# Performance work log

Hardware: AMD Instinct MI355X
Metric: run time of the kernel (lower is better)

Reference implementation:

```python
import jax, jax.numpy as jnp
import numpy as np

N_EMBD = 768
N_HEADS = 12
HEAD_DIM = N_EMBD // N_HEADS


def _layernorm(x):
    # LayerNorm without affine params, eps=1e-5 (torch default)
    mu = jnp.mean(x, axis=-1, keepdims=True)
    var = jnp.var(x, axis=-1, keepdims=True)
    return (x - mu) * jax.lax.rsqrt(var + 1e-5)


def setup_inputs() -> dict:
    key = jax.random.key(0)
    ks = jax.random.split(key, 6)
    B, T, C = 1, 4096, N_EMBD
    s = lambda fan_in: 1.0 / np.sqrt(fan_in)
    return {
        "x": jax.random.normal(ks[0], (B, T, C), jnp.float32),
        "W_kqv": jax.random.normal(ks[1], (C, 3 * C), jnp.float32) * s(C),
        "W_proj": jax.random.normal(ks[2], (C, C), jnp.float32) * s(C),
        "W_fc": jax.random.normal(ks[3], (C, 2 * C), jnp.float32) * s(C),
        "b_fc": jax.random.normal(ks[4], (2 * C,), jnp.float32) * s(C),
        "W_cproj": jax.random.normal(ks[5], (2 * C, C), jnp.float32) * s(2 * C),
    }


def _attention(h, W_kqv, W_proj):
    B, T, C = h.shape
    kqv = h @ W_kqv                       # (B, T, 3C)
    kqv = kqv.reshape(B, T, 3, N_HEADS, HEAD_DIM)
    k = kqv[:, :, 0]                      # (B, T, H, Dh) -- note k first, per source
    q = kqv[:, :, 1]
    v = kqv[:, :, 2]
    scale = HEAD_DIM ** -0.5
    scores = jnp.einsum('bqhd,bkhd->bhqk', q, k) * scale
    attn = jax.nn.softmax(scores, axis=-1)
    out = jnp.einsum('bhqk,bkhd->bqhd', attn, v).reshape(B, T, C)
    return out @ W_proj


def _mlp(h, W_fc, b_fc, W_cproj):
    h = h @ W_fc + b_fc
    h = jax.nn.gelu(h, approximate=False)  # torch nn.GELU default = exact erf
    return h @ W_cproj


def reference(x, W_kqv, W_proj, W_fc, b_fc, W_cproj):
    x = x + _attention(_layernorm(x), W_kqv, W_proj)
    x = x + _mlp(_layernorm(x), W_fc, b_fc, W_cproj)
    return x
```

## Files before the change

kernel.cpp:

```cpp
#include <hip/hip_runtime.h>
#include <hip/hip_bf16.h>
#include <math.h>

#define T_SEQ 4096
#define C_EMB 768
#define NHEAD 12
#define HDIM  64
#define NZ    2

typedef __bf16 bf16;
typedef __bf16 bf16x8 __attribute__((ext_vector_type(8)));
typedef __bf16 bf16x4 __attribute__((ext_vector_type(4)));
typedef float  f32x4  __attribute__((ext_vector_type(4)));
typedef float  f32x16 __attribute__((ext_vector_type(16)));

#if __has_builtin(__builtin_amdgcn_exp2f)
#define EXP2 __builtin_amdgcn_exp2f
#else
#define EXP2 exp2f
#endif


__device__ __forceinline__ void stage16(const void* g, void* ldsbase) {
  __builtin_amdgcn_global_load_lds(
      (__attribute__((address_space(1))) const unsigned int*)g,
      (__attribute__((address_space(3))) unsigned int*)ldsbase, 16, 0, 0);
}

__device__ __forceinline__ f32x16 zero16() {
  f32x16 z;
#pragma unroll
  for (int i = 0; i < 16; i++) z[i] = 0.f;
  return z;
}

__device__ __forceinline__ void do_transpose(const float* __restrict__ W,
                                             bf16* __restrict__ Wt, int K, int N,
                                             int bx, int by, int tid,
                                             float (*tile)[33]) {
  const int n0 = bx * 32, k0 = by * 32;
  const int tx = tid & 31, ty = tid >> 5;
#pragma unroll
  for (int i = 0; i < 32; i += 8)
    tile[ty + i][tx] = W[(size_t)(k0 + ty + i) * N + n0 + tx];
  __syncthreads();
#pragma unroll
  for (int i = 0; i < 32; i += 8)
    Wt[(size_t)(n0 + ty + i) * K + k0 + tx] = (bf16)tile[tx][ty + i];
}

__device__ __forceinline__ void do_ln(const float* __restrict__ x,
                                      bf16* __restrict__ y, int row, int t,
                                      float* red) {
  const float* xr = x + (size_t)row * C_EMB;
  float v0 = xr[t], v1 = xr[t + 256], v2 = xr[t + 512];
  float s  = v0 + v1 + v2;
  float ss = v0 * v0 + v1 * v1 + v2 * v2;
#pragma unroll
  for (int m = 1; m < 64; m <<= 1) {
    s += __shfl_xor(s, m);
    ss += __shfl_xor(ss, m);
  }
  const int w = t >> 6;
  if ((t & 63) == 0) { red[w] = s; red[4 + w] = ss; }
  __syncthreads();
  s  = red[0] + red[1] + red[2] + red[3];
  ss = red[4] + red[5] + red[6] + red[7];
  const float mu  = s * (1.0f / C_EMB);
  const float var = ss * (1.0f / C_EMB) - mu * mu;
  const float rs  = rsqrtf(var + 1e-5f);
  bf16* yr = y + (size_t)row * C_EMB;
  yr[t]       = (bf16)((v0 - mu) * rs);
  yr[t + 256] = (bf16)((v1 - mu) * rs);
  yr[t + 512] = (bf16)((v2 - mu) * rs);
}

__global__ void prep(const float* __restrict__ x, bf16* __restrict__ ln_out,
                     const float* __restrict__ W_kqv, bf16* __restrict__ Wkqv_t,
                     const float* __restrict__ W_proj, bf16* __restrict__ Wproj_t,
                     const float* __restrict__ W_fc, bf16* __restrict__ Wfc_t,
                     const float* __restrict__ W_cproj, bf16* __restrict__ Wcp_t) {
  __shared__ float tile[32][33];
  const int b = blockIdx.x, t = threadIdx.x;
  if (b < 1728) {
    do_transpose(W_kqv, Wkqv_t, 768, 2304, b % 72, b / 72, t, tile);
  } else if (b < 2304) {
    const int bb = b - 1728;
    do_transpose(W_proj, Wproj_t, 768, 768, bb % 24, bb / 24, t, tile);
  } else if (b < 3456) {
    const int bb = b - 2304;
    do_transpose(W_fc, Wfc_t, 768, 1536, bb % 48, bb / 48, t, tile);
  } else if (b < 4608) {
    const int bb = b - 3456;
    do_transpose(W_cproj, Wcp_t, 1536, 768, bb % 24, bb / 24, t, tile);
  } else {
    do_ln(x, ln_out, b - 4608, t, &tile[0][0]);
  }
}

__global__ void ln_rows(const bf16* __restrict__ x, bf16* __restrict__ y) {
  const int w = threadIdx.x >> 6, l = threadIdx.x & 63;
  const int row = blockIdx.x * 4 + w;
  const bf16* xr = x + (size_t)row * C_EMB;
  const bf16x8 v8 = *reinterpret_cast<const bf16x8*>(xr + l * 8);
  const bf16x4 v4 = *reinterpret_cast<const bf16x4*>(xr + 512 + l * 4);
  float f[12];
#pragma unroll
  for (int j = 0; j < 8; j++) f[j] = (float)v8[j];
#pragma unroll
  for (int j = 0; j < 4; j++) f[8 + j] = (float)v4[j];
  float s = 0.f, ss = 0.f;
#pragma unroll
  for (int j = 0; j < 12; j++) { s += f[j]; ss += f[j] * f[j]; }
#pragma unroll
  for (int m = 1; m < 64; m <<= 1) {
    s += __shfl_xor(s, m);
    ss += __shfl_xor(ss, m);
  }
  const float mu  = s * (1.0f / C_EMB);
  const float var = ss * (1.0f / C_EMB) - mu * mu;
  const float rs  = rsqrtf(var + 1e-5f);
  bf16x8 o8;
  bf16x4 o4;
#pragma unroll
  for (int j = 0; j < 8; j++) o8[j] = (bf16)((f[j] - mu) * rs);
#pragma unroll
  for (int j = 0; j < 4; j++) o4[j] = (bf16)((f[8 + j] - mu) * rs);
  bf16* yr = y + (size_t)row * C_EMB;
  *reinterpret_cast<bf16x8*>(yr + l * 8) = o8;
  *reinterpret_cast<bf16x4*>(yr + 512 + l * 4) = o4;
}

template <int EPI, int BM>
__global__ void gemm_bt(const bf16* __restrict__ A, const bf16* __restrict__ BT,
                        void* __restrict__ Cout, const void* __restrict__ res,
                        const float* __restrict__ bias, int M, int N, int K) {
  __shared__ __align__(16) bf16 As[BM * 64];
  __shared__ __align__(16) bf16 Bs[64 * 64];
  constexpr int MR = BM / 32;
  const int nrow = M / BM;
  const int ncol = N >> 6;
  const int rpx = nrow >> 3;
  const int bid = blockIdx.x;
  const int xcd = bid & 7, idx = bid >> 3;
  const int rowb = xcd * rpx + idx / ncol;
  const int colb = idx % ncol;
  const int row0 = rowb * BM, col0 = colb * 64;

  const int tid = threadIdx.x;
  const int w = tid >> 6, lane = tid & 63;
  const int wr = w >> 1, wc = w & 1;
  const int l15 = lane & 15, l4 = lane >> 4;

  f32x4 acc[MR][2];
#pragma unroll
  for (int m = 0; m < MR; m++)
#pragma unroll
    for (int n = 0; n < 2; n++) acc[m][n] = (f32x4){0.f, 0.f, 0.f, 0.f};

  const int rr = lane >> 3;
  const int c8 = (lane & 7) * 8;

  for (int k0 = 0; k0 < K; k0 += 64) {
    const bf16* gA = A + (size_t)(row0 + w * (BM / 4) + rr) * K + k0 + c8;
    const bf16* gB = BT + (size_t)(col0 + w * 16 + rr) * K + k0 + c8;
#pragma unroll
    for (int i = 0; i < BM / 32; i++)
      stage16(gA + (size_t)(8 * i) * K, As + (w * (BM / 4) + 8 * i) * 64);
#pragma unroll
    for (int i = 0; i < 2; i++)
      stage16(gB + (size_t)(8 * i) * K, Bs + (w * 16 + 8 * i) * 64);
    __syncthreads();

#pragma unroll
    for (int hh = 0; hh < 2; hh++) {
      bf16x8 af[MR], bfv[2];
#pragma unroll
      for (int m = 0; m < MR; m++)
        af[m] = *reinterpret_cast<const bf16x8*>(
            As + (wr * (BM / 2) + m * 16 + l15) * 64 + hh * 32 + l4 * 8);
#pragma unroll
      for (int n = 0; n < 2; n++)
        bfv[n] = *reinterpret_cast<const bf16x8*>(
            Bs + (wc * 32 + n * 16 + l15) * 64 + hh * 32 + l4 * 8);
#pragma unroll
      for (int m = 0; m < MR; m++)
#pragma unroll
        for (int n = 0; n < 2; n++)
          acc[m][n] = __builtin_amdgcn_mfma_f32_16x16x32_bf16(af[m], bfv[n], acc[m][n], 0, 0, 0);
    }
    __syncthreads();
  }

  const int orow = row0 + wr * (BM / 2);
  const int ocol = col0 + wc * 32;
#pragma unroll
  for (int m = 0; m < MR; m++) {
#pragma unroll
    for (int n = 0; n < 2; n++) {
      const int c = ocol + n * 16 + l15;
#pragma unroll
      for (int j = 0; j < 4; j++) {
        const int r = orow + m * 16 + l4 * 4 + j;
        const size_t idx2 = (size_t)r * N + c;
        const float v = acc[m][n][j];
        if (EPI == 0) {
          ((bf16*)Cout)[idx2] = (bf16)v;
        } else if (EPI == 1) {
          ((bf16*)Cout)[idx2] = (bf16)(((const float*)res)[idx2] + v);
        } else if (EPI == 2) {
          const float h = v + bias[c];
          ((bf16*)Cout)[idx2] = (bf16)(0.5f * h * (1.0f + erff(h * 0.70710678118f)));
        } else if (EPI == 3) {
          ((float*)Cout)[idx2] = (float)((const bf16*)res)[idx2] + v;
        } else {
          const float sc = (c >= 768 && c < 1536) ? 0.18033688011112042f : 1.0f;
          ((bf16*)Cout)[idx2] = (bf16)(v * sc);
        }
      }
    }
  }
}

__global__ __launch_bounds__(256, 3)
void attn_fused(const bf16* __restrict__ kqv,
                bf16* __restrict__ Opart,
                float* __restrict__ Lpart) {
  const int fid = blockIdx.x;
  const int xs = fid & 7, r = fid >> 3;
  const int qb = r & 31;
  const int s = xs * 3 + (r >> 5);
  const int h = s % 12, z = s / 12;
  const int tid = threadIdx.x, w = tid >> 6, lane = tid & 63;
  const int l31 = lane & 31, hi = lane >> 5;

  __shared__ __align__(16) char KsB[128 * 144];
  __shared__ __align__(16) char VtB[64 * 272];

  const int qrow = qb * 128 + w * 32 + l31;
  const bf16* qp = kqv + (size_t)qrow * 2304 + 768 + h * 64;
  bf16x8 qf[4];
#pragma unroll
  for (int m = 0; m < 4; m++)
    qf[m] = *reinterpret_cast<const bf16x8*>(qp + hi * 8 + 16 * m);

  bf16x8 ones;
#pragma unroll
  for (int e = 0; e < 8; e++) ones[e] = (bf16)1.0f;

  f32x16 accO0 = zero16(), accO1 = zero16(), accL = zero16();

  const int krow = tid >> 1;
  const int kc0 = (tid & 1) * 4;
  const int kb = tid & 31, db = tid >> 5;
  const int lb = ((kb >> 3) & 3) * 32 + ((kb >> 2) & 1) * 16 + (kb & 1) * 8 +
                 ((kb >> 1) & 1) * 4;

  const int kt0 = z * 16;

  bf16x8 kreg[4], vreg[4];
#define LOADKV(kt)                                                               \
  {                                                                              \
    const bf16* kp =                                                             \
        kqv + (size_t)((kt)*128 + krow) * 2304 + h * 64 + kc0 * 8;               \
    _Pragma("unroll") for (int i = 0; i < 4; i++)                                \
        kreg[i] = *reinterpret_cast<const bf16x8*>(kp + i * 8);                  \
    const bf16* vp =                                                             \
        kqv + (size_t)((kt)*128 + kb * 4) * 2304 + 1536 + h * 64 + db * 8;       \
    _Pragma("unroll") for (int r2 = 0; r2 < 4; r2++)                             \
        vreg[r2] = *reinterpret_cast<const bf16x8*>(vp + (size_t)r2 * 2304);     \
  }

  LOADKV(kt0);

  for (int kt = 0; kt < 16; kt++) {
    __syncthreads();
    {
      char* kdst = KsB + krow * 144;
#pragma unroll
      for (int i = 0; i < 4; i++)
        *reinterpret_cast<bf16x8*>(kdst + ((kc0 + i) * 16)) = kreg[i];
#pragma unroll
      for (int e = 0; e < 8; e++) {
        const int d = db * 8 + e;
        const bf16x4 pk4 = (bf16x4){vreg[0][e], vreg[1][e], vreg[2][e], vreg[3][e]};
        *reinterpret_cast<bf16x4*>(VtB + d * 272 + lb * 2) = pk4;
      }
    }
    __syncthreads();
    if (kt + 1 < 16) LOADKV(kt0 + kt + 1);

    __builtin_amdgcn_s_setprio(1);

    bf16x8 pb[8];
#pragma unroll
    for (int t = 0; t < 4; t++) {
      f32x16 st = zero16();
#pragma unroll
      for (int m = 0; m < 4; m++) {
        const bf16x8 kf = *reinterpret_cast<const bf16x8*>(
            KsB + (size_t)(32 * t + l31) * 144 + (2 * m + hi) * 16);
        st = __builtin_amdgcn_mfma_f32_32x32x16_bf16(kf, qf[m], st, 0, 0, 0);
      }
#pragma unroll
      for (int hf = 0; hf < 2; hf++) {
        bf16x8 p;
#pragma unroll
        for (int j = 0; j < 8; j++) p[j] = (bf16)EXP2(st[hf * 8 + j]);
        pb[2 * t + hf] = p;
      }
    }

#pragma unroll
    for (int mk = 0; mk < 8; mk++) {
      const bf16x8 vf0 = *reinterpret_cast<const bf16x8*>(
          VtB + (size_t)l31 * 272 + (2 * mk + hi) * 16);
      accO0 = __builtin_amdgcn_mfma_f32_32x32x16_bf16(vf0, pb[mk], accO0, 0, 0, 0);
      const bf16x8 vf1 = *reinterpret_cast<const bf16x8*>(
          VtB + (size_t)(32 + l31) * 272 + (2 * mk + hi) * 16);
      accO1 = __builtin_amdgcn_mfma_f32_32x32x16_bf16(vf1, pb[mk], accO1, 0, 0, 0);
      accL = __builtin_amdgcn_mfma_f32_32x32x16_bf16(ones, pb[mk], accL, 0, 0, 0);
    }

    __builtin_amdgcn_s_setprio(0);
  }
#undef LOADKV

  bf16* Oq = Opart + (size_t)z * T_SEQ * C_EMB + (size_t)qrow * C_EMB + h * 64;
#pragma unroll
  for (int s4 = 0; s4 < 4; s4++) {
    const bf16x4 o0 = (bf16x4){(bf16)accO0[4 * s4 + 0], (bf16)accO0[4 * s4 + 1],
                               (bf16)accO0[4 * s4 + 2], (bf16)accO0[4 * s4 + 3]};
    *reinterpret_cast<bf16x4*>(Oq + 8 * s4 + 4 * hi) = o0;
    const bf16x4 o1 = (bf16x4){(bf16)accO1[4 * s4 + 0], (bf16)accO1[4 * s4 + 1],
                               (bf16)accO1[4 * s4 + 2], (bf16)accO1[4 * s4 + 3]};
    *reinterpret_cast<bf16x4*>(Oq + 32 + 8 * s4 + 4 * hi) = o1;
  }
  if (hi == 0)
    Lpart[(size_t)z * NHEAD * T_SEQ + (size_t)h * T_SEQ + qrow] = accL[0];
}

__global__ void attn_combine(const bf16* __restrict__ Opart,
                             const float* __restrict__ Lpart,
                             bf16* __restrict__ out) {
  const int t = threadIdx.x;
  const int rr = t / 96, cc = t % 96;
  const int q = blockIdx.x * 4 + rr;
  const int c = cc * 8;
  const int h = c >> 6;
  float o[8];
#pragma unroll
  for (int j = 0; j < 8; j++) o[j] = 0.f;
  float L = 0.f;
#pragma unroll
  for (int z = 0; z < NZ; z++) {
    const bf16x8 v = *reinterpret_cast<const bf16x8*>(
        Opart + (size_t)z * T_SEQ * C_EMB + (size_t)q * C_EMB + c);
#pragma unroll
    for (int j = 0; j < 8; j++) o[j] += (float)v[j];
    L += Lpart[(size_t)z * NHEAD * T_SEQ + (size_t)h * T_SEQ + q];
  }
  const float inv = 1.0f / L;
  bf16x8 rv;
#pragma unroll
  for (int j = 0; j < 8; j++) rv[j] = (bf16)(o[j] * inv);
  *reinterpret_cast<bf16x8*>(out + (size_t)q * C_EMB + c) = rv;
}

extern "C" void kernel_launch(void* const* d_in, const int* in_sizes, int n_in,
                              void* d_out, int out_size, void* d_ws, size_t ws_size,
                              hipStream_t stream) {
  const float* x       = (const float*)d_in[0];
  const float* W_kqv   = (const float*)d_in[1];
  const float* W_proj  = (const float*)d_in[2];
  const float* W_fc    = (const float*)d_in[3];
  const float* b_fc    = (const float*)d_in[4];
  const float* W_cproj = (const float*)d_in[5];
  float* outp = (float*)d_out;

  char* p = (char*)d_ws;
  bf16* Wkqv_t  = (bf16*)p; p += (size_t)2304 * 768 * 2;
  bf16* Wproj_t = (bf16*)p; p += (size_t)768 * 768 * 2;
  bf16* Wfc_t   = (bf16*)p; p += (size_t)1536 * 768 * 2;
  bf16* Wcp_t   = (bf16*)p; p += (size_t)768 * 1536 * 2;
  bf16* A1      = (bf16*)p; p += (size_t)4096 * 768 * 2;
  bf16* KQV     = (bf16*)p; p += (size_t)4096 * 2304 * 2;
  bf16* x1      = (bf16*)p; p += (size_t)4096 * 768 * 2;
  bf16* Opart   = (bf16*)p; p += (size_t)NZ * 4096 * 768 * 2;
  float* Lpart  = (float*)p; p += (size_t)NZ * NHEAD * 4096 * 4;
  bf16* attn_o = A1;
  bf16* A2     = KQV;
  bf16* Hg     = KQV + (size_t)4096 * 768;

  prep<<<8704, 256, 0, stream>>>(x, A1, W_kqv, Wkqv_t, W_proj, Wproj_t,
                                 W_fc, Wfc_t, W_cproj, Wcp_t);
  gemm_bt<4, 128><<<1152, 256, 0, stream>>>(A1, Wkqv_t, KQV, nullptr, nullptr,
                                            4096, 2304, 768);
  attn_fused<<<768, 256, 0, stream>>>(KQV, Opart, Lpart);
  attn_combine<<<1024, 384, 0, stream>>>(Opart, Lpart, attn_o);
  gemm_bt<1, 64><<<768, 256, 0, stream>>>(attn_o, Wproj_t, x1, x, nullptr,
                                          4096, 768, 768);
  ln_rows<<<1024, 256, 0, stream>>>(x1, A2);
  gemm_bt<2, 64><<<1536, 256, 0, stream>>>(A2, Wfc_t, Hg, nullptr, b_fc,
                                           4096, 1536, 768);
  gemm_bt<3, 64><<<768, 256, 0, stream>>>(Hg, Wcp_t, outp, x1, nullptr,
                                          4096, 768, 1536);
}
```

Measured before the change: 178.3 us.

## Fuse attention split-combine into output projection GEMM prologue

Removes the separate attn_combine kernel and writes a dedicated projection GEMM that loads both partial attention outputs and their softmax denominators, sums and normalizes them while staging the A tile into LDS. This drops one launch and a full write and read of the combined attention output. In exchange the A operand is now loaded synchronously through registers rather than the async LDS path, and the new kernel has no double buffering, so the GEMM main loop may stall more.

New measurement: 178.0 us. Within noise of the previous version (-0.2%).

```diff
diff --git a/kernel.cpp b/kernel.cpp
--- a/kernel.cpp
+++ b/kernel.cpp
@@ -206,8 +206,6 @@
         const float v = acc[m][n][j];
         if (EPI == 0) {
           ((bf16*)Cout)[idx2] = (bf16)v;
-        } else if (EPI == 1) {
-          ((bf16*)Cout)[idx2] = (bf16)(((const float*)res)[idx2] + v);
         } else if (EPI == 2) {
           const float h = v + bias[c];
           ((bf16*)Cout)[idx2] = (bf16)(0.5f * h * (1.0f + erff(h * 0.70710678118f)));
@@ -217,6 +215,96 @@
           const float sc = (c >= 768 && c < 1536) ? 0.18033688011112042f : 1.0f;
           ((bf16*)Cout)[idx2] = (bf16)(v * sc);
         }
+      }
+    }
+  }
+}
+
+__global__ void gemm_proj(const bf16* __restrict__ Opart,
+                          const float* __restrict__ Lpart,
+                          const bf16* __restrict__ BT,
+                          bf16* __restrict__ Cout,
+                          const float* __restrict__ res) {
+  constexpr int M = 4096, N = 768, K = 768;
+  __shared__ __align__(16) bf16 As[64 * 64];
+  __shared__ __align__(16) bf16 Bs[64 * 64];
+  const int bid = blockIdx.x;
+  const int xcd = bid & 7, idx = bid >> 3;
+  const int rowb = xcd * 8 + idx / 12;
+  const int colb = idx % 12;
+  const int row0 = rowb * 64, col0 = colb * 64;
+
+  const int tid = threadIdx.x;
+  const int w = tid >> 6, lane = tid & 63;
+  const int wr = w >> 1, wc = w & 1;
+  const int l15 = lane & 15, l4 = lane >> 4;
+
+  f32x4 acc[2][2];
+#pragma unroll
+  for (int m = 0; m < 2; m++)
+#pragma unroll
+    for (int n = 0; n < 2; n++) acc[m][n] = (f32x4){0.f, 0.f, 0.f, 0.f};
+
+  const int rr = lane >> 3;
+  const int c8 = (lane & 7) * 8;
+
+  for (int k0 = 0; k0 < K; k0 += 64) {
+    const int h = k0 >> 6;
+#pragma unroll
+    for (int i = 0; i < 2; i++) {
+      const int ar = row0 + w * 16 + 8 * i + rr;
+      const float L =
+          Lpart[(size_t)h * T_SEQ + ar] +
+          Lpart[(size_t)NHEAD * T_SEQ + (size_t)h * T_SEQ + ar];
+      const float inv = 1.0f / L;
+      const bf16x8 o0 = *reinterpret_cast<const bf16x8*>(
+          Opart + (size_t)ar * C_EMB + k0 + c8);
+      const bf16x8 o1 = *reinterpret_cast<const bf16x8*>(
+          Opart + (size_t)T_SEQ * C_EMB + (size_t)ar * C_EMB + k0 + c8);
+      bf16x8 av;
+#pragma unroll
+      for (int j = 0; j < 8; j++)
+        av[j] = (bf16)(((float)o0[j] + (float)o1[j]) * inv);
+      *reinterpret_cast<bf16x8*>(As + (w * 16 + 8 * i + rr) * 64 + c8) = av;
+    }
+    const bf16* gB = BT + (size_t)(col0 + w * 16 + rr) * K + k0 + c8;
+#pragma unroll
+    for (int i = 0; i < 2; i++)
+      stage16(gB + (size_t)(8 * i) * K, Bs + (w * 16 + 8 * i) * 64);
+    __syncthreads();
+
+#pragma unroll
+    for (int hh = 0; hh < 2; hh++) {
+      bf16x8 af[2], bfv[2];
+#pragma unroll
+      for (int m = 0; m < 2; m++)
+        af[m] = *reinterpret_cast<const bf16x8*>(
+            As + (wr * 32 + m * 16 + l15) * 64 + hh * 32 + l4 * 8);
+#pragma unroll
+      for (int n = 0; n < 2; n++)
+        bfv[n] = *reinterpret_cast<const bf16x8*>(
+            Bs + (wc * 32 + n * 16 + l15) * 64 + hh * 32 + l4 * 8);
+#pragma unroll
+      for (int m = 0; m < 2; m++)
+#pragma unroll
+        for (int n = 0; n < 2; n++)
+          acc[m][n] = __builtin_amdgcn_mfma_f32_16x16x32_bf16(af[m], bfv[n], acc[m][n], 0, 0, 0);
+    }
+    __syncthreads();
+  }
+
+  const int orow = row0 + wr * 32;
+  const int ocol = col0 + wc * 32;
+#pragma unroll
+  for (int m = 0; m < 2; m++) {
+#pragma unroll
+    for (int n = 0; n < 2; n++) {
+      const int c = ocol + n * 16 + l15;
+#pragma unroll
+      for (int j = 0; j < 4; j++) {
+        const int r = orow + m * 16 + l4 * 4 + j;
+        const size_t idx2 = (size_t)r * N + c;
+        Cout[idx2] = (bf16)(res[idx2] + acc[m][n][j]);
       }
     }
   }
@@ -340,33 +428,6 @@
     Lpart[(size_t)z * NHEAD * T_SEQ + (size_t)h * T_SEQ + qrow] = accL[0];
 }
 
-__global__ void attn_combine(const bf16* __restrict__ Opart,
-                             const float* __restrict__ Lpart,
-                             bf16* __restrict__ out) {
-  const int t = threadIdx.x;
-  const int rr = t / 96, cc = t % 96;
-  const int q = blockIdx.x * 4 + rr;
-  const int c = cc * 8;
-  const int h = c >> 6;
-  float o[8];
-#pragma unroll
-  for (int j = 0; j < 8; j++) o[j] = 0.f;
-  float L = 0.f;
-#pragma unroll
-  for (int z = 0; z < NZ; z++) {
-    const bf16x8 v = *reinterpret_cast<const bf16x8*>(
-        Opart + (size_t)z * T_SEQ * C_EMB + (size_t)q * C_EMB + c);
-#pragma unroll
-    for (int j = 0; j < 8; j++) o[j] += (float)v[j];
-    L += Lpart[(size_t)z * NHEAD * T_SEQ + (size_t)h * T_SEQ + q];
-  }
-  const float inv = 1.0f / L;
-  bf16x8 rv;
-#pragma unroll
-  for (int j = 0; j < 8; j++) rv[j] = (bf16)(o[j] * inv);
-  *reinterpret_cast<bf16x8*>(out + (size_t)q * C_EMB + c) = rv;
-}
-
 extern "C" void kernel_launch(void* const* d_in, const int* in_sizes, int n_in,
                               void* d_out, int out_size, void* d_ws, size_t ws_size,
                               hipStream_t stream) {
@@ -388,7 +449,6 @@
   bf16* x1      = (bf16*)p; p += (size_t)4096 * 768 * 2;
   bf16* Opart   = (bf16*)p; p += (size_t)NZ * 4096 * 768 * 2;
   float* Lpart  = (float*)p; p += (size_t)NZ * NHEAD * 4096 * 4;
-  bf16* attn_o = A1;
   bf16* A2     = KQV;
   bf16* Hg     = KQV + (size_t)4096 * 768;
 
@@ -397,9 +457,7 @@
   gemm_bt<4, 128><<<1152, 256, 0, stream>>>(A1, Wkqv_t, KQV, nullptr, nullptr,
                                             4096, 2304, 768);
   attn_fused<<<768, 256, 0, stream>>>(KQV, Opart, Lpart);
-  attn_combine<<<1024, 384, 0, stream>>>(Opart, Lpart, attn_o);
-  gemm_bt<1, 64><<<768, 256, 0, stream>>>(attn_o, Wproj_t, x1, x, nullptr,
-                                          4096, 768, 768);
+  gemm_proj<<<768, 256, 0, stream>>>(Opart, Lpart, Wproj_t, x1, x);
   ln_rows<<<1024, 256, 0, stream>>>(x1, A2);
   gemm_bt<2, 64><<<1536, 256, 0, stream>>>(A2, Wfc_t, Hg, nullptr, b_fc,
                                            4096, 1536, 768);
```
